# Kernel tuning notes

Hardware: AMD Instinct MI355X
Metric: run time of the kernel (lower is better)

The kernel has to match this reference:

```python
import jax, jax.numpy as jnp
import numpy as np

N, E, IN, HID, H, OUT = 10000, 160000, 256, 64, 8, 16
NEG_SLOPE = 0.2  # PyG GATConv leaky_relu slope


def _layer_norm(x, g, b, eps=1e-5):
    m = x.mean(-1, keepdims=True)
    v = ((x - m) ** 2).mean(-1, keepdims=True)
    return (x - m) * jax.lax.rsqrt(v + eps) * g + b


def _gat_conv(x, src, dst, W, a_src, a_dst, bias, concat):
    # PyG GATConv: h = x @ W -> [N,H,C]; e_ij = leakyrelu(a_src.h_j + a_dst.h_i);
    # alpha = segment-softmax over incoming edges at dst; out_i = sum_j alpha_ij h_j
    n = x.shape[0]
    heads, c = a_src.shape
    h = (x @ W).reshape(n, heads, c)
    al_s = (h * a_src[None]).sum(-1)  # [N,H]
    al_d = (h * a_dst[None]).sum(-1)  # [N,H]
    e = al_s[src] + al_d[dst]         # [Etot,H]
    e = jnp.where(e > 0, e, NEG_SLOPE * e)
    m = jax.ops.segment_max(e, dst, num_segments=n)
    p = jnp.exp(e - m[dst])
    s = jax.ops.segment_sum(p, dst, num_segments=n)
    a = p / (s[dst] + 1e-16)          # [Etot,H]
    out = jax.ops.segment_sum(h[src] * a[:, :, None], dst, num_segments=n)
    out = out.reshape(n, heads * c) if concat else out.mean(axis=1)
    return out + bias


def setup_inputs() -> dict:
    key = jax.random.key(0)
    ks = jax.random.split(key, 12)
    d = {}
    d['x'] = jax.random.normal(ks[0], (N, IN), jnp.float32)
    d['edge_index'] = jax.random.randint(ks[1], (2, E), 0, N, jnp.int64)
    d['Wp'] = jax.random.normal(ks[2], (IN, HID * H), jnp.float32) * 0.05
    d['bp'] = jnp.zeros((HID * H,), jnp.float32)
    d['g0'] = jnp.ones((HID * H,), jnp.float32)
    d['b0'] = jnp.zeros((HID * H,), jnp.float32)
    d['W1'] = jax.random.normal(ks[3], (HID * H, HID * H), jnp.float32) * 0.05
    d['as1'] = jax.random.normal(ks[4], (H, HID), jnp.float32) * 0.1
    d['ad1'] = jax.random.normal(ks[5], (H, HID), jnp.float32) * 0.1
    d['b1'] = jnp.zeros((HID * H,), jnp.float32)
    d['g1'] = jnp.ones((HID * H,), jnp.float32)
    d['be1'] = jnp.zeros((HID * H,), jnp.float32)
    d['W2'] = jax.random.normal(ks[6], (HID * H, HID * H), jnp.float32) * 0.05
    d['as2'] = jax.random.normal(ks[7], (H, HID), jnp.float32) * 0.1
    d['ad2'] = jax.random.normal(ks[8], (H, HID), jnp.float32) * 0.1
    d['b2'] = jnp.zeros((HID * H,), jnp.float32)
    d['g2'] = jnp.ones((HID * H,), jnp.float32)
    d['be2'] = jnp.zeros((HID * H,), jnp.float32)
    d['W3'] = jax.random.normal(ks[9], (HID * H, OUT), jnp.float32) * 0.05
    d['as3'] = jax.random.normal(ks[10], (1, OUT), jnp.float32) * 0.1
    d['ad3'] = jax.random.normal(ks[11], (1, OUT), jnp.float32) * 0.1
    d['b3'] = jnp.zeros((OUT,), jnp.float32)
    d['g3'] = jnp.ones((OUT,), jnp.float32)
    d['be3'] = jnp.zeros((OUT,), jnp.float32)
    return d


def reference(x, edge_index, Wp, bp, g0, b0, W1, as1, ad1, b1, g1, be1,
              W2, as2, ad2, b2, g2, be2, W3, as3, ad3, b3, g3, be3):
    n = x.shape[0]
    loops = jnp.arange(n)  # PyG add_self_loops=True
    src = jnp.concatenate([edge_index[0], loops])
    dst = jnp.concatenate([edge_index[1], loops])
    x = jax.nn.elu(_layer_norm(x @ Wp + bp, g0, b0))
    # layer 1 (heads=8, concat) + residual
    r = x
    x = _gat_conv(x, src, dst, W1, as1, ad1, b1, True)
    x = jax.nn.elu(_layer_norm(x, g1, be1)) + r
    # layer 2 (heads=8, concat) + residual
    r = x
    x = _gat_conv(x, src, dst, W2, as2, ad2, b2, True)
    x = jax.nn.elu(_layer_norm(x, g2, be2)) + r
    # final layer (heads=1, mean/no-concat), no elu/residual
    x = _gat_conv(x, src, dst, W3, as3, ad3, b3, False)
    x = _layer_norm(x, g3, be3)
    return x
```

## Files before the change

### kernel.cpp

```cpp
#include <hip/hip_runtime.h>
#include <hip/hip_bf16.h>

#define NNODES 10000
#define NEDGES 160000
#define ETOT   (NEDGES + NNODES)
#define CIN    256
#define CH     512
#define NHEAD  8
#define HDIM   64
#define COUT   16
#define NEG_SLOPE 0.2f
#define NF ((size_t)NNODES * CH)

__device__ __forceinline__ float bf2f(uint u) {
    union { uint i; float f; } v; v.i = u << 16; return v.f;
}
__device__ __forceinline__ ushort f2bf(float x) {
    union { float f; uint i; } v; v.f = x;
    uint r = v.i + 0x7fff + ((v.i >> 16) & 1);
    return (ushort)(r >> 16);
}

typedef __attribute__((ext_vector_type(8))) short short8v;
typedef __attribute__((ext_vector_type(4))) float f32x4;

__global__ void count_deg_k(const int* __restrict__ ei, int* __restrict__ deg) {
    int eid = blockIdx.x * 256 + threadIdx.x;
    if (eid >= ETOT) return;
    int dst = (eid < NEDGES) ? ei[NEDGES + eid] : (eid - NEDGES);
    atomicAdd(&deg[dst], 1);
}

__global__ __launch_bounds__(512) void scan_k(const int* __restrict__ deg, int* __restrict__ startA) {
    __shared__ int partial[512];
    int t = threadIdx.x;
    const int per = (NNODES + 511) / 512;
    int base = t * per;
    int s = 0;
    for (int j = 0; j < per; ++j) { int idx = base + j; if (idx < NNODES) s += deg[idx]; }
    partial[t] = s;
    __syncthreads();
    for (int off = 1; off < 512; off <<= 1) {
        int v = (t >= off) ? partial[t - off] : 0;
        __syncthreads();
        partial[t] += v;
        __syncthreads();
    }
    int run = (t == 0) ? 0 : partial[t - 1];
    for (int j = 0; j < per; ++j) {
        int idx = base + j;
        if (idx < NNODES) { startA[idx] = run; run += deg[idx]; }
    }
}

__global__ void scatter_k(const int* __restrict__ ei, const int* __restrict__ startA,
                          int* __restrict__ cursor, int* __restrict__ csr_src) {
    int eid = blockIdx.x * 256 + threadIdx.x;
    if (eid >= ETOT) return;
    int src, dst;
    if (eid < NEDGES) { src = ei[eid]; dst = ei[NEDGES + eid]; }
    else { src = dst = eid - NEDGES; }
    int pos = startA[dst] + atomicAdd(&cursor[dst], 1);
    csr_src[pos] = src;
}

__global__ void convert_x_k(const float* __restrict__ x, ushort* __restrict__ xb) {
    int idx = blockIdx.x * 256 + threadIdx.x;
    if (idx >= NNODES * CIN / 4) return;
    float4 v = ((const float4*)x)[idx];
    ushort4 o; o.x = f2bf(v.x); o.y = f2bf(v.y); o.z = f2bf(v.z); o.w = f2bf(v.w);
    ((ushort4*)xb)[idx] = o;
}

__global__ __launch_bounds__(256) void convert_wT_k(const float* __restrict__ W, ushort* __restrict__ Wt,
                                                    int K, int N) {
    __shared__ float tile[32][33];
    int tx = threadIdx.x & 31, ty = threadIdx.x >> 5;
    int n0 = blockIdx.x * 32, k0 = blockIdx.y * 32;
#pragma unroll
    for (int r = 0; r < 32; r += 8)
        tile[ty + r][tx] = W[(size_t)(k0 + ty + r) * N + n0 + tx];
    __syncthreads();
#pragma unroll
    for (int r = 0; r < 32; r += 8)
        Wt[(size_t)(n0 + ty + r) * K + k0 + tx] = f2bf(tile[tx][ty + r]);
}

#define LDB 72
__global__ __launch_bounds__(256) void gemm_mfma(const ushort* __restrict__ A, const ushort* __restrict__ Bt,
                                                 const float* __restrict__ bias, ushort* __restrict__ C,
                                                 const float* __restrict__ a_src, const float* __restrict__ a_dst,
                                                 float* __restrict__ als, float* __restrict__ ald,
                                                 int M, int K) {
    __shared__ ushort Asl[64 * LDB];
    __shared__ ushort Bsl[64 * LDB];
    __shared__ float lals[2][64], lald[2][64];
    int t = threadIdx.x;
    int wid = t >> 6, lane = t & 63;
    int row0 = blockIdx.x * 64, col0 = blockIdx.y * 64;
    int wr = (wid >> 1) * 32, wc = (wid & 1) * 32;
    f32x4 acc[2][2] = {};
    int sRow = t >> 2;
    int sK = (t & 3) * 16;
    int lr = lane & 15;
    int kg = lane >> 4;

    for (int k0 = 0; k0 < K; k0 += 64) {
        int gr = row0 + sRow;
        uint4 av0 = {0u,0u,0u,0u}, av1 = {0u,0u,0u,0u};
        if (gr < M) {
            const ushort* ap = A + (size_t)gr * K + k0 + sK;
            av0 = *(const uint4*)ap; av1 = *(const uint4*)(ap + 8);
        }
        *(uint4*)(&Asl[sRow * LDB + sK]) = av0;
        *(uint4*)(&Asl[sRow * LDB + sK + 8]) = av1;
        const ushort* bp = Bt + (size_t)(col0 + sRow) * K + k0 + sK;
        *(uint4*)(&Bsl[sRow * LDB + sK]) = *(const uint4*)bp;
        *(uint4*)(&Bsl[sRow * LDB + sK + 8]) = *(const uint4*)(bp + 8);
        __syncthreads();
#pragma unroll
        for (int ks = 0; ks < 2; ++ks) {
            short8v a0 = *(const short8v*)&Asl[(wr + lr) * LDB + ks * 32 + kg * 8];
            short8v a1 = *(const short8v*)&Asl[(wr + 16 + lr) * LDB + ks * 32 + kg * 8];
            short8v b0 = *(const short8v*)&Bsl[(wc + lr) * LDB + ks * 32 + kg * 8];
            short8v b1 = *(const short8v*)&Bsl[(wc + 16 + lr) * LDB + ks * 32 + kg * 8];
            acc[0][0] = __builtin_amdgcn_mfma_f32_16x16x32_bf16(a0, b0, acc[0][0], 0, 0, 0);
            acc[0][1] = __builtin_amdgcn_mfma_f32_16x16x32_bf16(a0, b1, acc[0][1], 0, 0, 0);
            acc[1][0] = __builtin_amdgcn_mfma_f32_16x16x32_bf16(a1, b0, acc[1][0], 0, 0, 0);
            acc[1][1] = __builtin_amdgcn_mfma_f32_16x16x32_bf16(a1, b1, acc[1][1], 0, 0, 0);
        }
        __syncthreads();
    }
    float pals[2][4] = {}, pald[2][4] = {};
    bool doLog = (a_src != nullptr);
    int head = blockIdx.y;
#pragma unroll
    for (int i = 0; i < 2; ++i) {
#pragma unroll
        for (int j = 0; j < 2; ++j) {
            int cl = wc + j * 16 + lr;
            int c = col0 + cl;
            float bb = bias ? bias[c] : 0.f;
            float as_c = doLog ? a_src[head * HDIM + cl] : 0.f;
            float ad_c = doLog ? a_dst[head * HDIM + cl] : 0.f;
#pragma unroll
            for (int q = 0; q < 4; ++q) {
                int r = row0 + wr + i * 16 + kg * 4 + q;
                float hv = acc[i][j][q] + bb;
                if (r < M) C[(size_t)r * CH + c] = f2bf(hv);
                pals[i][q] += hv * as_c;
                pald[i][q] += hv * ad_c;
            }
        }
    }
    if (doLog) {
#pragma unroll
        for (int i = 0; i < 2; ++i)
#pragma unroll
            for (int q = 0; q < 4; ++q) {
#pragma unroll
                for (int off = 1; off < 16; off <<= 1) {
                    pals[i][q] += __shfl_xor(pals[i][q], off);
                    pald[i][q] += __shfl_xor(pald[i][q], off);
                }
            }
        if (lr == 0) {
#pragma unroll
            for (int i = 0; i < 2; ++i)
#pragma unroll
                for (int q = 0; q < 4; ++q) {
                    int r = wr + i * 16 + kg * 4 + q;
                    lals[wid & 1][r] = pals[i][q];
                    lald[wid & 1][r] = pald[i][q];
                }
        }
        __syncthreads();
        if (t < 64) {
            int r = row0 + t;
            if (r < M) {
                als[r * NHEAD + head] = lals[0][t] + lals[1][t];
                ald[r * NHEAD + head] = lald[0][t] + lald[1][t];
            }
        }
    }
}

__global__ __launch_bounds__(128) void ln_elu_k(const ushort* __restrict__ inb, const float* __restrict__ g,
                                                const float* __restrict__ b, ushort* __restrict__ outb) {
    int i = blockIdx.x, t = threadIdx.x;
    uint2 hv = ((const uint2*)(inb + (size_t)i * CH))[t];
    float a0 = bf2f(hv.x & 0xffff), a1 = bf2f(hv.x >> 16);
    float a2 = bf2f(hv.y & 0xffff), a3 = bf2f(hv.y >> 16);
    float s = a0 + a1 + a2 + a3;
    float s2 = a0 * a0 + a1 * a1 + a2 * a2 + a3 * a3;
#pragma unroll
    for (int off = 1; off < 64; off <<= 1) { s += __shfl_xor(s, off); s2 += __shfl_xor(s2, off); }
    __shared__ float sh[4];
    int wid = t >> 6, lane = t & 63;
    if (lane == 0) { sh[wid] = s; sh[2 + wid] = s2; }
    __syncthreads();
    float tot = sh[0] + sh[1], tot2 = sh[2] + sh[3];
    float mean = tot * (1.0f / CH);
    float var = tot2 * (1.0f / CH) - mean * mean;
    float rstd = rsqrtf(var + 1e-5f);
    float4 gv = ((const float4*)g)[t];
    float4 bv = ((const float4*)b)[t];
    float y0 = (a0 - mean) * rstd * gv.x + bv.x; y0 = y0 > 0.f ? y0 : __expf(y0) - 1.f;
    float y1 = (a1 - mean) * rstd * gv.y + bv.y; y1 = y1 > 0.f ? y1 : __expf(y1) - 1.f;
    float y2 = (a2 - mean) * rstd * gv.z + bv.z; y2 = y2 > 0.f ? y2 : __expf(y2) - 1.f;
    float y3 = (a3 - mean) * rstd * gv.w + bv.w; y3 = y3 > 0.f ? y3 : __expf(y3) - 1.f;
    ushort4 o; o.x = f2bf(y0); o.y = f2bf(y1); o.z = f2bf(y2); o.w = f2bf(y3);
    ((ushort4*)(outb + (size_t)i * CH))[t] = o;
}

__global__ __launch_bounds__(128) void agg_ln_k(const ushort* __restrict__ hb, const float* __restrict__ als,
                                                const float* __restrict__ ald, const int* __restrict__ startA,
                                                const int* __restrict__ deg, const int* __restrict__ csr,
                                                const float* __restrict__ bias, const float* __restrict__ gamma,
                                                const float* __restrict__ beta, const ushort* __restrict__ residb,
                                                ushort* __restrict__ outb) {
    int t = threadIdx.x;
    int i = blockIdx.x * 2 + (t >> 6);
    int tl = t & 63;
    int c0 = tl * 8, head = tl >> 3;
    int s0 = startA[i], d = deg[i];
    float aldv = ald[i * NHEAD + head];
    const int* cp = csr + s0;
    float m = -1e30f;
    for (int e = 0; e < d; ++e) {
        int src = cp[e];
        float ee = als[src * NHEAD + head] + aldv;
        ee = ee > 0.f ? ee : NEG_SLOPE * ee;
        m = fmaxf(m, ee);
    }
    float ssum = 0.f;
    float a0 = 0, a1 = 0, a2 = 0, a3 = 0, a4 = 0, a5 = 0, a6 = 0, a7 = 0;
    for (int e = 0; e < d; ++e) {
        int src = cp[e];
        float ee = als[src * NHEAD + head] + aldv;
        ee = ee > 0.f ? ee : NEG_SLOPE * ee;
        float p = __expf(ee - m);
        ssum += p;
        uint4 hv = *(const uint4*)(hb + (size_t)src * CH + c0);
        a0 += p * bf2f(hv.x & 0xffff); a1 += p * bf2f(hv.x >> 16);
        a2 += p * bf2f(hv.y & 0xffff); a3 += p * bf2f(hv.y >> 16);
        a4 += p * bf2f(hv.z & 0xffff); a5 += p * bf2f(hv.z >> 16);
        a6 += p * bf2f(hv.w & 0xffff); a7 += p * bf2f(hv.w >> 16);
    }
    float inv = 1.0f / (ssum + 1e-16f);
    float4 bi0 = ((const float4*)bias)[tl * 2], bi1 = ((const float4*)bias)[tl * 2 + 1];
    a0 = a0 * inv + bi0.x; a1 = a1 * inv + bi0.y; a2 = a2 * inv + bi0.z; a3 = a3 * inv + bi0.w;
    a4 = a4 * inv + bi1.x; a5 = a5 * inv + bi1.y; a6 = a6 * inv + bi1.z; a7 = a7 * inv + bi1.w;
    float s = a0 + a1 + a2 + a3 + a4 + a5 + a6 + a7;
    float s2 = a0*a0 + a1*a1 + a2*a2 + a3*a3 + a4*a4 + a5*a5 + a6*a6 + a7*a7;
#pragma unroll
    for (int off = 1; off < 64; off <<= 1) { s += __shfl_xor(s, off); s2 += __shfl_xor(s2, off); }
    float mean = s * (1.0f / CH);
    float var = s2 * (1.0f / CH) - mean * mean;
    float rstd = rsqrtf(var + 1e-5f);
    float4 gv0 = ((const float4*)gamma)[tl * 2], gv1 = ((const float4*)gamma)[tl * 2 + 1];
    float4 bv0 = ((const float4*)beta)[tl * 2],  bv1 = ((const float4*)beta)[tl * 2 + 1];
    uint4 rv = ((const uint4*)(residb + (size_t)i * CH))[tl];
    float y0 = (a0 - mean) * rstd * gv0.x + bv0.x; y0 = (y0 > 0.f ? y0 : __expf(y0) - 1.f) + bf2f(rv.x & 0xffff);
    float y1 = (a1 - mean) * rstd * gv0.y + bv0.y; y1 = (y1 > 0.f ? y1 : __expf(y1) - 1.f) + bf2f(rv.x >> 16);
    float y2 = (a2 - mean) * rstd * gv0.z + bv0.z; y2 = (y2 > 0.f ? y2 : __expf(y2) - 1.f) + bf2f(rv.y & 0xffff);
    float y3 = (a3 - mean) * rstd * gv0.w + bv0.w; y3 = (y3 > 0.f ? y3 : __expf(y3) - 1.f) + bf2f(rv.y >> 16);
    float y4 = (a4 - mean) * rstd * gv1.x + bv1.x; y4 = (y4 > 0.f ? y4 : __expf(y4) - 1.f) + bf2f(rv.z & 0xffff);
    float y5 = (a5 - mean) * rstd * gv1.y + bv1.y; y5 = (y5 > 0.f ? y5 : __expf(y5) - 1.f) + bf2f(rv.z >> 16);
    float y6 = (a6 - mean) * rstd * gv1.z + bv1.z; y6 = (y6 > 0.f ? y6 : __expf(y6) - 1.f) + bf2f(rv.w & 0xffff);
    float y7 = (a7 - mean) * rstd * gv1.w + bv1.w; y7 = (y7 > 0.f ? y7 : __expf(y7) - 1.f) + bf2f(rv.w >> 16);
    uint4 o;
    o.x = (uint)f2bf(y0) | ((uint)f2bf(y1) << 16);
    o.y = (uint)f2bf(y2) | ((uint)f2bf(y3) << 16);
    o.z = (uint)f2bf(y4) | ((uint)f2bf(y5) << 16);
    o.w = (uint)f2bf(y6) | ((uint)f2bf(y7) << 16);
    ((uint4*)(outb + (size_t)i * CH))[tl] = o;
}

__global__ __launch_bounds__(256) void gemm_small_k(const ushort* __restrict__ A, const float* __restrict__ W,
                                                    float* __restrict__ C) {
    int col = threadIdx.x & 15;
    int row = blockIdx.x * 16 + (threadIdx.x >> 4);
    if (row >= NNODES) return;
    const ushort* ar = A + (size_t)row * CH;
    float acc = 0.f;
#pragma unroll 8
    for (int k = 0; k < CH; k += 2) {
        uint av = *(const uint*)(ar + k);
        acc += bf2f(av & 0xffff) * W[k * COUT + col];
        acc += bf2f(av >> 16) * W[(k + 1) * COUT + col];
    }
    C[row * COUT + col] = acc;
}

__global__ __launch_bounds__(256) void agg16f_k(const float* __restrict__ h3, const float* __restrict__ as3,
                                                const float* __restrict__ ad3, const int* __restrict__ startA,
                                                const int* __restrict__ deg, const int* __restrict__ csr,
                                                const float* __restrict__ b3, const float* __restrict__ g3,
                                                const float* __restrict__ be3, float* __restrict__ out) {
    int t = threadIdx.x;
    int i = blockIdx.x * 16 + (t >> 4);
    int c = t & 15;
    if (i >= NNODES) return;
    float asc = as3[c], adc = ad3[c];
    float ald_i = h3[i * COUT + c] * adc;
#pragma unroll
    for (int off = 1; off < 16; off <<= 1) ald_i += __shfl_xor(ald_i, off, 16);
    int s0 = startA[i], d = deg[i];
    float m = -1e30f;
    for (int e = 0; e < d; ++e) {
        int src = csr[s0 + e];
        float al = h3[src * COUT + c] * asc;
#pragma unroll
        for (int off = 1; off < 16; off <<= 1) al += __shfl_xor(al, off, 16);
        float ee = al + ald_i;
        ee = ee > 0.f ? ee : NEG_SLOPE * ee;
        m = fmaxf(m, ee);
    }
    float ssum = 0.f, acc = 0.f;
    for (int e = 0; e < d; ++e) {
        int src = csr[s0 + e];
        float v = h3[src * COUT + c];
        float al = v * asc;
#pragma unroll
        for (int off = 1; off < 16; off <<= 1) al += __shfl_xor(al, off, 16);
        float ee = al + ald_i;
        ee = ee > 0.f ? ee : NEG_SLOPE * ee;
        float p = __expf(ee - m);
        ssum += p;
        acc += p * v;
    }
    acc = acc / (ssum + 1e-16f) + b3[c];
    float v = acc, v2 = acc * acc;
#pragma unroll
    for (int off = 1; off < 16; off <<= 1) { v += __shfl_xor(v, off, 16); v2 += __shfl_xor(v2, off, 16); }
    float mean = v * (1.0f / COUT);
    float var = v2 * (1.0f / COUT) - mean * mean;
    out[i * COUT + c] = (acc - mean) * rsqrtf(var + 1e-5f) * g3[c] + be3[c];
}

extern "C" void kernel_launch(void* const* d_in, const int* in_sizes, int n_in,
                              void* d_out, int out_size, void* d_ws, size_t ws_size,
                              hipStream_t stream) {
    const float* x   = (const float*)d_in[0];
    const int*   ei  = (const int*)d_in[1];
    const float* Wp  = (const float*)d_in[2];
    const float* bp  = (const float*)d_in[3];
    const float* g0  = (const float*)d_in[4];
    const float* b0  = (const float*)d_in[5];
    const float* W1  = (const float*)d_in[6];
    const float* as1 = (const float*)d_in[7];
    const float* ad1 = (const float*)d_in[8];
    const float* b1  = (const float*)d_in[9];
    const float* g1  = (const float*)d_in[10];
    const float* be1 = (const float*)d_in[11];
    const float* W2  = (const float*)d_in[12];
    const float* as2 = (const float*)d_in[13];
    const float* ad2 = (const float*)d_in[14];
    const float* b2  = (const float*)d_in[15];
    const float* g2  = (const float*)d_in[16];
    const float* be2 = (const float*)d_in[17];
    const float* W3  = (const float*)d_in[18];
    const float* as3 = (const float*)d_in[19];
    const float* ad3 = (const float*)d_in[20];
    const float* b3  = (const float*)d_in[21];
    const float* g3  = (const float*)d_in[22];
    const float* be3 = (const float*)d_in[23];

    ushort* B0  = (ushort*)d_ws;
    ushort* B1  = B0 + NF;
    ushort* B2  = B1 + NF;
    ushort* xbf = B2 + NF;
    ushort* Wpt = xbf + (size_t)NNODES * CIN;
    ushort* W1t = Wpt + (size_t)CIN * CH;
    ushort* W2t = W1t + (size_t)CH * CH;
    float* als = (float*)(W2t + (size_t)CH * CH);
    float* ald = als + NNODES * NHEAD;
    float* h3  = ald + NNODES * NHEAD;
    int* deg = (int*)(h3 + (size_t)NNODES * COUT);
    int* stA = deg + NNODES;
    int* cur = stA + NNODES;
    int* csr = cur + NNODES;

    hipMemsetAsync(deg, 0, NNODES * sizeof(int), stream);
    hipMemsetAsync(cur, 0, NNODES * sizeof(int), stream);
    count_deg_k<<<(ETOT + 255) / 256, 256, 0, stream>>>(ei, deg);
    scan_k<<<1, 512, 0, stream>>>(deg, stA);
    scatter_k<<<(ETOT + 255) / 256, 256, 0, stream>>>(ei, stA, cur, csr);

    convert_x_k<<<(NNODES * CIN / 4 + 255) / 256, 256, 0, stream>>>(x, xbf);
    convert_wT_k<<<dim3(CH / 32, CIN / 32), 256, 0, stream>>>(Wp, Wpt, CIN, CH);
    convert_wT_k<<<dim3(CH / 32, CH / 32), 256, 0, stream>>>(W1, W1t, CH, CH);
    convert_wT_k<<<dim3(CH / 32, CH / 32), 256, 0, stream>>>(W2, W2t, CH, CH);

    dim3 gg((NNODES + 63) / 64, CH / 64);

    gemm_mfma<<<gg, 256, 0, stream>>>(xbf, Wpt, bp, B0, nullptr, nullptr, nullptr, nullptr, NNODES, CIN);
    ln_elu_k<<<NNODES, 128, 0, stream>>>(B0, g0, b0, B1);

    gemm_mfma<<<gg, 256, 0, stream>>>(B1, W1t, nullptr, B2, as1, ad1, als, ald, NNODES, CH);
    agg_ln_k<<<NNODES / 2, 128, 0, stream>>>(B2, als, ald, stA, deg, csr, b1, g1, be1, B1, B0);

    gemm_mfma<<<gg, 256, 0, stream>>>(B0, W2t, nullptr, B1, as2, ad2, als, ald, NNODES, CH);
    agg_ln_k<<<NNODES / 2, 128, 0, stream>>>(B1, als, ald, stA, deg, csr, b2, g2, be2, B0, B2);

    gemm_small_k<<<(NNODES + 15) / 16, 256, 0, stream>>>(B2, W3, h3);
    agg16f_k<<<(NNODES + 15) / 16, 256, 0, stream>>>(h3, as3, ad3, stA, deg, csr, b3, g3, be3, (float*)d_out);
}
```

Baseline: 349.4 us.

## Split each node's edge aggregation across four waves with shared-memory reduction

The GAT aggregation kernel now assigns one node per 256-thread block and strides the incoming edges across four wavefronts instead of one wavefront per node. Partial softmax maxima, sums and 8-wide feature accumulators are combined through shared memory with two block barriers, and only wave 0 finishes the layer norm, ELU, residual and store. The aim is more memory-level parallelism on the latency-bound gather of neighbour rows (average degree about 17). In exchange it adds barriers, shared-memory traffic, redundant final reductions in waves 1 to 3, and leaves three quarters of the threads idle in the epilogue.

```diff
diff --git a/kernel.cpp b/kernel.cpp
--- a/kernel.cpp
+++ b/kernel.cpp
@@ -213,29 +213,35 @@
     ((ushort4*)(outb + (size_t)i * CH))[t] = o;
 }
 
-__global__ __launch_bounds__(128) void agg_ln_k(const ushort* __restrict__ hb, const float* __restrict__ als,
+__global__ __launch_bounds__(256) void agg_ln_k(const ushort* __restrict__ hb, const float* __restrict__ als,
                                                 const float* __restrict__ ald, const int* __restrict__ startA,
                                                 const int* __restrict__ deg, const int* __restrict__ csr,
                                                 const float* __restrict__ bias, const float* __restrict__ gamma,
                                                 const float* __restrict__ beta, const ushort* __restrict__ residb,
                                                 ushort* __restrict__ outb) {
+    __shared__ float mws[4][8];
+    __shared__ float sws[4][8];
+    __shared__ float accb[4][8][64];
     int t = threadIdx.x;
-    int i = blockIdx.x * 2 + (t >> 6);
-    int tl = t & 63;
+    int w = t >> 6, tl = t & 63;
+    int i = blockIdx.x;
     int c0 = tl * 8, head = tl >> 3;
     int s0 = startA[i], d = deg[i];
     float aldv = ald[i * NHEAD + head];
     const int* cp = csr + s0;
     float m = -1e30f;
-    for (int e = 0; e < d; ++e) {
+    for (int e = w; e < d; e += 4) {
         int src = cp[e];
         float ee = als[src * NHEAD + head] + aldv;
         ee = ee > 0.f ? ee : NEG_SLOPE * ee;
         m = fmaxf(m, ee);
     }
+    if ((tl & 7) == 0) mws[w][head] = m;
+    __syncthreads();
+    m = fmaxf(fmaxf(mws[0][head], mws[1][head]), fmaxf(mws[2][head], mws[3][head]));
     float ssum = 0.f;
     float a0 = 0, a1 = 0, a2 = 0, a3 = 0, a4 = 0, a5 = 0, a6 = 0, a7 = 0;
-    for (int e = 0; e < d; ++e) {
+    for (int e = w; e < d; e += 4) {
         int src = cp[e];
         float ee = als[src * NHEAD + head] + aldv;
         ee = ee > 0.f ? ee : NEG_SLOPE * ee;
@@ -247,6 +253,19 @@
         a4 += p * bf2f(hv.z & 0xffff); a5 += p * bf2f(hv.z >> 16);
         a6 += p * bf2f(hv.w & 0xffff); a7 += p * bf2f(hv.w >> 16);
     }
+    if ((tl & 7) == 0) sws[w][head] = ssum;
+    accb[w][0][tl] = a0; accb[w][1][tl] = a1; accb[w][2][tl] = a2; accb[w][3][tl] = a3;
+    accb[w][4][tl] = a4; accb[w][5][tl] = a5; accb[w][6][tl] = a6; accb[w][7][tl] = a7;
+    __syncthreads();
+    ssum = sws[0][head] + sws[1][head] + sws[2][head] + sws[3][head];
+    a0 = accb[0][0][tl] + accb[1][0][tl] + accb[2][0][tl] + accb[3][0][tl];
+    a1 = accb[0][1][tl] + accb[1][1][tl] + accb[2][1][tl] + accb[3][1][tl];
+    a2 = accb[0][2][tl] + accb[1][2][tl] + accb[2][2][tl] + accb[3][2][tl];
+    a3 = accb[0][3][tl] + accb[1][3][tl] + accb[2][3][tl] + accb[3][3][tl];
+    a4 = accb[0][4][tl] + accb[1][4][tl] + accb[2][4][tl] + accb[3][4][tl];
+    a5 = accb[0][5][tl] + accb[1][5][tl] + accb[2][5][tl] + accb[3][5][tl];
+    a6 = accb[0][6][tl] + accb[1][6][tl] + accb[2][6][tl] + accb[3][6][tl];
+    a7 = accb[0][7][tl] + accb[1][7][tl] + accb[2][7][tl] + accb[3][7][tl];
     float inv = 1.0f / (ssum + 1e-16f);
     float4 bi0 = ((const float4*)bias)[tl * 2], bi1 = ((const float4*)bias)[tl * 2 + 1];
     a0 = a0 * inv + bi0.x; a1 = a1 * inv + bi0.y; a2 = a2 * inv + bi0.z; a3 = a3 * inv + bi0.w;
@@ -255,6 +274,7 @@
     float s2 = a0*a0 + a1*a1 + a2*a2 + a3*a3 + a4*a4 + a5*a5 + a6*a6 + a7*a7;
 #pragma unroll
     for (int off = 1; off < 64; off <<= 1) { s += __shfl_xor(s, off); s2 += __shfl_xor(s2, off); }
+    if (w != 0) return;
     float mean = s * (1.0f / CH);
     float var = s2 * (1.0f / CH) - mean * mean;
     float rstd = rsqrtf(var + 1e-5f);
@@ -399,10 +419,10 @@
     ln_elu_k<<<NNODES, 128, 0, stream>>>(B0, g0, b0, B1);
 
     gemm_mfma<<<gg, 256, 0, stream>>>(B1, W1t, nullptr, B2, as1, ad1, als, ald, NNODES, CH);
-    agg_ln_k<<<NNODES / 2, 128, 0, stream>>>(B2, als, ald, stA, deg, csr, b1, g1, be1, B1, B0);
+    agg_ln_k<<<NNODES, 256, 0, stream>>>(B2, als, ald, stA, deg, csr, b1, g1, be1, B1, B0);
 
     gemm_mfma<<<gg, 256, 0, stream>>>(B0, W2t, nullptr, B1, as2, ad2, als, ald, NNODES, CH);
-    agg_ln_k<<<NNODES / 2, 128, 0, stream>>>(B1, als, ald, stA, deg, csr, b2, g2, be2, B0, B2);
+    agg_ln_k<<<NNODES, 256, 0, stream>>>(B1, als, ald, stA, deg, csr, b2, g2, be2, B0, B2);
 
     gemm_small_k<<<(NNODES + 15) / 16, 256, 0, stream>>>(B2, W3, h3);
     agg16f_k<<<(NNODES + 15) / 16, 256, 0, stream>>>(h3, as3, ad3, stA, deg, csr, b3, g3, be3, (float*)d_out);
```

After: 343.2 us. No clear change (-1.8%).
